# Kernel optimization log

Hardware: AMD Instinct MI355X
Metric: run time of the kernel (lower is better)

## Reference

```python
import jax, jax.numpy as jnp
import numpy as np

DIM = 1024
NH = 16
HD = DIM // NH  # 64
WINDOW = 8      # window_size; flash window=(WINDOW-1, -1) with causal=True
EPS_NORM = 1e-6


def _rmsnorm(h, w):
    # RMSNorm over last dim (full model dim, applied before head split)
    return h * jax.lax.rsqrt(jnp.mean(h * h, axis=-1, keepdims=True) + EPS_NORM) * w


def _rope(h, cos, sin):
    # h: [bv, L, NH, HD]; cos/sin: [L, HD//2]; torch view-as-complex pairs adjacent elems
    hr = h[..., 0::2]
    hi = h[..., 1::2]
    c = cos[None, :, None, :]
    s = sin[None, :, None, :]
    out_r = hr * c - hi * s
    out_i = hr * s + hi * c
    return jnp.stack([out_r, out_i], axis=-1).reshape(h.shape)


def setup_inputs() -> dict:
    key = jax.random.key(0)
    ks = jax.random.split(key, 8)
    bv, f, nlt = 1, 16, 1472
    b = bv * f
    L = f * nlt
    wscale = DIM ** -0.5
    x = jax.random.normal(ks[0], (b, nlt, DIM), jnp.float32)
    # standard RoPE tables, base 10000, d//2 frequencies
    pos = jnp.arange(L, dtype=jnp.float32)[:, None]
    inv_freq = 1.0 / (10000.0 ** (jnp.arange(HD // 2, dtype=jnp.float32) / (HD // 2)))
    ang = pos * inv_freq[None, :]
    inp = {
        'x': x,
        'freqs_cos': jnp.cos(ang),
        'freqs_sin': jnp.sin(ang),
        'q_w': jax.random.normal(ks[1], (DIM, DIM), jnp.float32) * wscale,
        'q_b': jnp.zeros((DIM,), jnp.float32),
        'k_w': jax.random.normal(ks[2], (DIM, DIM), jnp.float32) * wscale,
        'k_b': jnp.zeros((DIM,), jnp.float32),
        'v_w': jax.random.normal(ks[3], (DIM, DIM), jnp.float32) * wscale,
        'v_b': jnp.zeros((DIM,), jnp.float32),
        'o_w': jax.random.normal(ks[4], (DIM, DIM), jnp.float32) * wscale,
        'o_b': jnp.zeros((DIM,), jnp.float32),
        'norm_q_w': jnp.ones((DIM,), jnp.float32),
        'norm_k_w': jnp.ones((DIM,), jnp.float32),
        'bv': 1,
        'f': 16,
        'nlt': 1472,
    }
    return inp


def reference(x, freqs_cos, freqs_sin, q_w, q_b, k_w, k_b, v_w, v_b, o_w, o_b,
              norm_q_w, norm_k_w, bv, f, nlt):
    b, s = x.shape[:2]  # b = bv*f, s = nlt
    q = _rmsnorm(x @ q_w.T + q_b, norm_q_w)
    k = _rmsnorm(x @ k_w.T + k_b, norm_k_w)
    v = (x @ v_w.T + v_b).reshape(bv, f, s, NH, HD)
    # RoPE over flattened (frame, token) positions
    q4 = q.reshape(bv, f * s, NH, HD)
    k4 = k.reshape(bv, f * s, NH, HD)
    qr = _rope(q4, freqs_cos, freqs_sin)
    kr = _rope(k4, freqs_cos, freqs_sin)
    # temporal layout: [bv*nlt, f, NH, HD] (attend over frames per latent token)
    qr = qr.reshape(bv, f, s, NH, HD).transpose(0, 2, 1, 3, 4).reshape(bv * s, f, NH, HD)
    kr = kr.reshape(bv, f, s, NH, HD).transpose(0, 2, 1, 3, 4).reshape(bv * s, f, NH, HD)
    vr = v.transpose(0, 2, 1, 3, 4).reshape(bv * s, f, NH, HD)
    # causal sliding-window mask over frames: j <= i and i - j < WINDOW
    fi = jnp.arange(f)
    mask = (fi[None, :] <= fi[:, None]) & (fi[:, None] - fi[None, :] < WINDOW)  # [f, f]
    scores = jnp.einsum('bqhd,bkhd->bhqk', qr, kr) / np.float32(np.sqrt(HD))
    scores = jnp.where(mask[None, None], scores, jnp.float32(-1e30))
    attn = jax.nn.softmax(scores, axis=-1)
    o = jnp.einsum('bhqk,bkhd->bqhd', attn, vr)  # [bv*nlt, f, NH, HD]
    o = o.reshape(bv, s, f, NH, HD).transpose(0, 2, 1, 3, 4).reshape(bv * f, s, DIM)
    return o @ o_w.T + o_b
```

## Files before the change

kernel.cpp:

```cpp
#include <hip/hip_runtime.h>
#include <hip/hip_bf16.h>
#include <math.h>

typedef __bf16 bf16;
typedef bf16 bf16x8 __attribute__((ext_vector_type(8)));
typedef bf16 bf16x4 __attribute__((ext_vector_type(4)));
typedef float f32x4 __attribute__((ext_vector_type(4)));

#define NFRM 16
#define SEQ  1472
#define TOK  (NFRM * SEQ)
#define DIM_ 1024
#define NH_  16
#define HD_  64
#define KROW 1032


__device__ __forceinline__ void load_lds_16B(const void* g, void* l) {
  __builtin_amdgcn_global_load_lds(
      (const __attribute__((address_space(1))) unsigned int*)g,
      (__attribute__((address_space(3))) unsigned int*)l,
      16, 0, 0);
}

__global__ __launch_bounds__(256) void cvt_bf16(const float* __restrict__ s,
                                                bf16* __restrict__ d, int n) {
  size_t i = ((size_t)blockIdx.x * 256 + threadIdx.x) * 8;
  if (i >= (size_t)n) return;
  const int r   = (int)(i >> 10);
  const int col = (int)(i & 1023);
  const int f   = r / SEQ;
  const int t   = r - f * SEQ;
  const size_t o = ((size_t)(t * 16 + f) << 10) + col;
  f32x4 a = *(const f32x4*)(s + i);
  f32x4 b = *(const f32x4*)(s + i + 4);
  bf16x8 v;
  v[0] = (bf16)a[0]; v[1] = (bf16)a[1]; v[2] = (bf16)a[2]; v[3] = (bf16)a[3];
  v[4] = (bf16)b[0]; v[5] = (bf16)b[1]; v[6] = (bf16)b[2]; v[7] = (bf16)b[3];
  *(bf16x8*)(d + o) = v;
}

__global__ __launch_bounds__(256) void cvt_w4(
    const float* __restrict__ w0, const float* __restrict__ w1,
    const float* __restrict__ w2, const float* __restrict__ w3,
    bf16* __restrict__ d0, bf16* __restrict__ d1,
    bf16* __restrict__ d2, bf16* __restrict__ d3) {
  const int z = blockIdx.y;
  const float* s = (z == 0) ? w0 : (z == 1) ? w1 : (z == 2) ? w2 : w3;
  bf16* d       = (z == 0) ? d0 : (z == 1) ? d1 : (z == 2) ? d2 : d3;
  size_t i = ((size_t)blockIdx.x * 256 + threadIdx.x) * 8;
  f32x4 a = *(const f32x4*)(s + i);
  f32x4 b = *(const f32x4*)(s + i + 4);
  bf16x8 o;
  o[0] = (bf16)a[0]; o[1] = (bf16)a[1]; o[2] = (bf16)a[2]; o[3] = (bf16)a[3];
  o[4] = (bf16)b[0]; o[5] = (bf16)b[1]; o[6] = (bf16)b[2]; o[7] = (bf16)b[3];
  *(bf16x8*)(d + i) = o;
}

__device__ __forceinline__ void swz368(int h, int& bx, int& by) {
  const int s = (h & 7) * 46 + (h >> 3);
  bx = s >> 2;
  by = s & 3;
}

template <typename OutT, int OMAP>
__device__ __forceinline__ void gemm256_body(const bf16* __restrict__ A,
                                             const bf16* __restrict__ B,
                                             const float* __restrict__ bias,
                                             OutT* __restrict__ C,
                                             bf16* lds, int bx, int by) {
  const int tid  = threadIdx.x;
  const int w    = tid >> 6;
  const int lane = tid & 63;
  const int am0  = bx * 256;
  const int bn0  = by * 256;

  const int rstep = w * 8 + (lane >> 3);
  const int jsrc  = ((lane & 7) ^ ((lane >> 3) & 7)) * 8;
  const int arb[4] = {0, 128, 64, 192};
  const bf16* srcp[8];
  int dstoff[8];
#pragma unroll
  for (int s = 0; s < 4; ++s) {
    srcp[s]   = B + (size_t)(bn0 + s * 64 + rstep) * DIM_ + jsrc;
    dstoff[s] = 32768 + s * 8192 + w * 1024;
    srcp[4 + s]   = A + (size_t)(am0 + arb[s] + rstep) * DIM_ + jsrc;
    dstoff[4 + s] = arb[s] * 128 + w * 1024;
  }

  const int wr   = w >> 2;
  const int wc   = w & 3;
  const int frow = lane & 15;
  const int g    = lane >> 4;
  const int sw   = (frow & 7) << 4;
  const int e0   = (g * 16) ^ sw;
  const int e1   = (g * 16 + 64) ^ sw;
  const int aA   = (wr * 128 + frow) * 128;
  const int bB   = 32768 + (wc * 64 + frow) * 128;

  f32x4 acc[8][4];
#pragma unroll
  for (int i = 0; i < 8; ++i)
#pragma unroll
    for (int j = 0; j < 4; ++j) {
      f32x4 z = {0.f, 0.f, 0.f, 0.f};
      acc[i][j] = z;
    }

  char* ldsc = (char*)lds;

#pragma unroll
  for (int s = 0; s < 8; ++s) load_lds_16B(srcp[s], ldsc + dstoff[s]);

#pragma unroll 1
  for (int it = 0; it < 8; ++it) {
#pragma unroll
    for (int half = 0; half < 2; ++half) {
      const int kt   = it * 2 + half;
      const int cur  = half ? 65536 : 0;
      const int nxt  = half ? 0 : 65536;
      const int kpre = (kt < 15) ? (kt + 1) * 64 : 15 * 64;

      asm volatile("s_waitcnt vmcnt(2)" ::: "memory");
      asm volatile("s_barrier" ::: "memory");
#pragma unroll
      for (int s = 0; s < 4; ++s)
        load_lds_16B(srcp[s] + kpre, ldsc + nxt + dstoff[s]);

      bf16x8 bfv[4][2];
#pragma unroll
      for (int j = 0; j < 4; ++j) {
        bfv[j][0] = *(const bf16x8*)(ldsc + cur + bB + j * 2048 + e0);
        bfv[j][1] = *(const bf16x8*)(ldsc + cur + bB + j * 2048 + e1);
      }

#pragma unroll
      for (int p = 0; p < 4; ++p) {
        if (p == 1) {
          load_lds_16B(srcp[4] + kpre, ldsc + nxt + dstoff[4]);
          load_lds_16B(srcp[5] + kpre, ldsc + nxt + dstoff[5]);
        }
        if (p == 2) {
          asm volatile("s_waitcnt vmcnt(6)" ::: "memory");
          asm volatile("s_barrier" ::: "memory");
          load_lds_16B(srcp[6] + kpre, ldsc + nxt + dstoff[6]);
          load_lds_16B(srcp[7] + kpre, ldsc + nxt + dstoff[7]);
        }
        bf16x8 af[2][2];
#pragma unroll
        for (int ii = 0; ii < 2; ++ii) {
          const int i = p * 2 + ii;
          af[ii][0] = *(const bf16x8*)(ldsc + cur + aA + i * 2048 + e0);
          af[ii][1] = *(const bf16x8*)(ldsc + cur + aA + i * 2048 + e1);
        }
        __builtin_amdgcn_s_setprio(1);
#pragma unroll
        for (int ii = 0; ii < 2; ++ii) {
          const int i = p * 2 + ii;
#pragma unroll
          for (int j = 0; j < 4; ++j) {
            acc[i][j] = __builtin_amdgcn_mfma_f32_16x16x32_bf16(
                af[ii][0], bfv[j][0], acc[i][j], 0, 0, 0);
            acc[i][j] = __builtin_amdgcn_mfma_f32_16x16x32_bf16(
                af[ii][1], bfv[j][1], acc[i][j], 0, 0, 0);
          }
        }
        __builtin_amdgcn_s_setprio(0);
      }
    }
  }

  const int cl = lane & 15;
  const int rq = g * 4;
#pragma unroll
  for (int j = 0; j < 4; ++j) {
    const int nc   = bn0 + wc * 64 + j * 16 + cl;
    const float bb = bias[nc];
#pragma unroll
    for (int i = 0; i < 8; ++i) {
#pragma unroll
      for (int r = 0; r < 4; ++r) {
        const int rowp = am0 + wr * 128 + i * 16 + rq + r;
        const size_t mr = (OMAP == 1)
            ? ((size_t)(rowp & 15) * SEQ + (rowp >> 4))
            : (size_t)rowp;
        C[mr * DIM_ + nc] = (OutT)(acc[i][j][r] + bb);
      }
    }
  }
}

__global__ __launch_bounds__(512, 2) void gemm_qkv(
    const bf16* __restrict__ A,
    const bf16* __restrict__ Bq, const bf16* __restrict__ Bk,
    const bf16* __restrict__ Bv,
    const float* __restrict__ bq, const float* __restrict__ bk,
    const float* __restrict__ bv,
    bf16* __restrict__ Cq, bf16* __restrict__ Ck, bf16* __restrict__ Cv) {
  __shared__ __align__(16) bf16 lds[65536];
  const int z = blockIdx.z;
  const bf16* B    = (z == 0) ? Bq : (z == 1) ? Bk : Bv;
  const float* bia = (z == 0) ? bq : (z == 1) ? bk : bv;
  bf16* C          = (z == 0) ? Cq : (z == 1) ? Ck : Cv;
  int bx, by;
  swz368(blockIdx.y * 92 + blockIdx.x, bx, by);
  gemm256_body<bf16, 0>(A, B, bia, C, lds, bx, by);
}

__global__ __launch_bounds__(512, 2) void gemm_out(
    const bf16* __restrict__ A, const bf16* __restrict__ B,
    const float* __restrict__ bias, float* __restrict__ C) {
  __shared__ __align__(16) bf16 lds[65536];
  int bx, by;
  swz368(blockIdx.y * 92 + blockIdx.x, bx, by);
  gemm256_body<float, 1>(A, B, bias, C, lds, bx, by);
}

__global__ __launch_bounds__(512, 4) void attn_win(
    const bf16* __restrict__ q, const bf16* __restrict__ k,
    const bf16* __restrict__ v, bf16* __restrict__ o,
    const float* __restrict__ nqw, const float* __restrict__ nkw,
    const float* __restrict__ fcos, const float* __restrict__ fsin) {
  __shared__ __align__(16) bf16 ks[16 * KROW];
  __shared__ __align__(16) bf16 xs[16 * KROW];
  __shared__ __align__(16) bf16 ps[16 * 256];
  const int t    = blockIdx.x;
  const int tid  = threadIdx.x;
  const int wave = tid >> 6, lane = tid & 63;
  const size_t tb = (size_t)t * (16 * DIM_);

  const bf16* vg = v + tb + (size_t)tid * 32;
  bf16x8 vr0 = *(const bf16x8*)(vg);
  bf16x8 vr1 = *(const bf16x8*)(vg + 8);
  bf16x8 vr2 = *(const bf16x8*)(vg + 16);
  bf16x8 vr3 = *(const bf16x8*)(vg + 24);

#pragma unroll
  for (int i = 0; i < 4; ++i) {
    const int j = wave * 4 + i;
    const int r = j >> 1, half = j & 1;
    const size_t g = tb + (size_t)r * DIM_ + half * 512 + lane * 8;
    load_lds_16B(k + g, ks + r * KROW + half * 512);
    load_lds_16B(q + g, xs + r * KROW + half * 512);
  }
  __syncthreads();

#pragma unroll
  for (int i = 0; i < 4; ++i) {
    const int m  = wave * 4 + i;
    const int fr = m & 15;
    bf16* rowp = ((m < 16) ? xs : ks) + fr * KROW;
    const float* nw = (m < 16) ? nqw : nkw;
    bf16x8 a = *(const bf16x8*)(rowp + lane * 8);
    bf16x8 b = *(const bf16x8*)(rowp + 512 + lane * 8);
    float xa[8], xb[8];
    float ssq = 0.f;
#pragma unroll
    for (int e = 0; e < 8; ++e) {
      xa[e] = (float)a[e]; xb[e] = (float)b[e];
      ssq += xa[e] * xa[e] + xb[e] * xb[e];
    }
#pragma unroll
    for (int off = 32; off > 0; off >>= 1) ssq += __shfl_xor(ssq, off);
    const float rs = rsqrtf(ssq * (1.0f / 1024.0f) + 1e-6f);
    float wA[8], wB[8];
    f32x4 w0 = *(const f32x4*)(nw + lane * 8);
    f32x4 w1 = *(const f32x4*)(nw + lane * 8 + 4);
    f32x4 w2 = *(const f32x4*)(nw + 512 + lane * 8);
    f32x4 w3 = *(const f32x4*)(nw + 512 + lane * 8 + 4);
#pragma unroll
    for (int e = 0; e < 4; ++e) {
      wA[e] = w0[e]; wA[4 + e] = w1[e];
      wB[e] = w2[e]; wB[4 + e] = w3[e];
    }
    const size_t pos = (size_t)fr * SEQ + t;
    f32x4 cc = *(const f32x4*)(fcos + pos * 32 + (lane & 7) * 4);
    f32x4 sn = *(const f32x4*)(fsin + pos * 32 + (lane & 7) * 4);
    bf16x8 oa, ob;
#pragma unroll
    for (int p = 0; p < 4; ++p) {
      const float a0 = xa[2 * p] * rs * wA[2 * p];
      const float a1 = xa[2 * p + 1] * rs * wA[2 * p + 1];
      const float b0 = xb[2 * p] * rs * wB[2 * p];
      const float b1 = xb[2 * p + 1] * rs * wB[2 * p + 1];
      oa[2 * p]     = (bf16)(a0 * cc[p] - a1 * sn[p]);
      oa[2 * p + 1] = (bf16)(a0 * sn[p] + a1 * cc[p]);
      ob[2 * p]     = (bf16)(b0 * cc[p] - b1 * sn[p]);
      ob[2 * p + 1] = (bf16)(b0 * sn[p] + b1 * cc[p]);
    }
    *(bf16x8*)(rowp + lane * 8)       = oa;
    *(bf16x8*)(rowp + 512 + lane * 8) = ob;
  }
  __syncthreads();

  const int fl  = lane & 15;
  const int kq  = (lane >> 4) * 8;
#pragma unroll
  for (int hh = 0; hh < 2; ++hh) {
    const int h = wave * 2 + hh;
    const int qo = fl * KROW + h * HD_ + kq;
    bf16x8 aq0 = *(const bf16x8*)(xs + qo);
    bf16x8 aq1 = *(const bf16x8*)(xs + qo + 32);
    bf16x8 bk0 = *(const bf16x8*)(ks + qo);
    bf16x8 bk1 = *(const bf16x8*)(ks + qo + 32);
    f32x4 sc = {0.f, 0.f, 0.f, 0.f};
    sc = __builtin_amdgcn_mfma_f32_16x16x32_bf16(aq0, bk0, sc, 0, 0, 0);
    sc = __builtin_amdgcn_mfma_f32_16x16x32_bf16(aq1, bk1, sc, 0, 0, 0);
#pragma unroll
    for (int r = 0; r < 4; ++r) {
      const int row = (lane >> 4) * 4 + r;
      const bool valid = (fl <= row) && (row - fl < 8);
      float s = valid ? sc[r] * 0.125f : -1e30f;
      float m = s;
#pragma unroll
      for (int off = 8; off > 0; off >>= 1) m = fmaxf(m, __shfl_xor(m, off));
      const float e = __expf(s - m);
      float su = e;
#pragma unroll
      for (int off = 8; off > 0; off >>= 1) su += __shfl_xor(su, off);
      ps[h * 256 + row * 16 + fl] = (bf16)(e / su);
    }
  }
  __syncthreads();

  {
    bf16* vd = xs + (tid >> 5) * KROW + (tid & 31) * 32;
    *(bf16x8*)(vd)      = vr0;
    *(bf16x8*)(vd + 8)  = vr1;
    *(bf16x8*)(vd + 16) = vr2;
    *(bf16x8*)(vd + 24) = vr3;
  }
  __syncthreads();

  const int h3 = tid >> 5;
  const int dc = (tid >> 2) & 7;
  const int fg = tid & 3;
  bf16x8 pr[8];
#pragma unroll
  for (int i = 0; i < 4; ++i) {
    pr[2 * i]     = *(const bf16x8*)(ps + h3 * 256 + (fg * 4 + i) * 16);
    pr[2 * i + 1] = *(const bf16x8*)(ps + h3 * 256 + (fg * 4 + i) * 16 + 8);
  }
  float acc[4][8];
#pragma unroll
  for (int i = 0; i < 4; ++i)
#pragma unroll
    for (int d = 0; d < 8; ++d) acc[i][d] = 0.f;

  const bf16* vb = xs + h3 * HD_ + dc * 8;
#pragma unroll
  for (int fk2 = 0; fk2 < 16; ++fk2) {
    bf16x8 vv8 = *(const bf16x8*)(vb + fk2 * KROW);
    float vf[8];
#pragma unroll
    for (int d = 0; d < 8; ++d) vf[d] = (float)vv8[d];
#pragma unroll
    for (int i = 0; i < 4; ++i) {
      const float pp = (float)((fk2 < 8) ? pr[2 * i][fk2] : pr[2 * i + 1][fk2 - 8]);
#pragma unroll
      for (int d = 0; d < 8; ++d) acc[i][d] += pp * vf[d];
    }
  }
#pragma unroll
  for (int i = 0; i < 4; ++i) {
    bf16x8 ov;
#pragma unroll
    for (int d = 0; d < 8; ++d) ov[d] = (bf16)acc[i][d];
    *(bf16x8*)(o + tb + (size_t)(fg * 4 + i) * DIM_ + h3 * HD_ + dc * 8) = ov;
  }
}

extern "C" void kernel_launch(void* const* d_in, const int* in_sizes, int n_in,
                              void* d_out, int out_size, void* d_ws,
                              size_t ws_size, hipStream_t stream) {
  const float* x    = (const float*)d_in[0];
  const float* fcos = (const float*)d_in[1];
  const float* fsin = (const float*)d_in[2];
  const float* q_w  = (const float*)d_in[3];
  const float* q_b  = (const float*)d_in[4];
  const float* k_w  = (const float*)d_in[5];
  const float* k_b  = (const float*)d_in[6];
  const float* v_w  = (const float*)d_in[7];
  const float* v_b  = (const float*)d_in[8];
  const float* o_w  = (const float*)d_in[9];
  const float* o_b  = (const float*)d_in[10];
  const float* nqw  = (const float*)d_in[11];
  const float* nkw  = (const float*)d_in[12];
  float* out = (float*)d_out;

  char* ws = (char*)d_ws;
  const size_t SZ  = (size_t)TOK * DIM_ * 2;
  const size_t WSZ = (size_t)DIM_ * DIM_ * 2;
  bf16* xb = (bf16*)(ws);
  bf16* wq = (bf16*)(ws + SZ);
  bf16* wk = (bf16*)(ws + SZ + WSZ);
  bf16* wv = (bf16*)(ws + SZ + 2 * WSZ);
  bf16* wo = (bf16*)(ws + SZ + 3 * WSZ);
  bf16* qq = (bf16*)(ws + SZ + 4 * WSZ);
  bf16* kk = (bf16*)(ws + SZ + 4 * WSZ + SZ);
  bf16* vv = (bf16*)(ws + SZ + 4 * WSZ + 2 * SZ);
  bf16* om = xb;

  const int NTOT = TOK * DIM_;
  const int NW   = DIM_ * DIM_;

  cvt_bf16<<<NTOT / 2048, 256, 0, stream>>>(x, xb, NTOT);
  cvt_w4<<<dim3(NW / 2048, 4), 256, 0, stream>>>(q_w, k_w, v_w, o_w,
                                                 wq, wk, wv, wo);

  dim3 gq(TOK / 256, DIM_ / 256, 3);
  gemm_qkv<<<gq, 512, 0, stream>>>(xb, wq, wk, wv, q_b, k_b, v_b, qq, kk, vv);

  attn_win<<<SEQ, 512, 0, stream>>>(qq, kk, vv, om, nqw, nkw, fcos, fsin);

  gemm_out<<<dim3(TOK / 256, DIM_ / 256), 512, 0, stream>>>(om, wo, o_b, out);
}
```

Measured before the change: 505.3 us.

## Use 128x128 tiles for output GEMM and unify QKV tile swizzle

Replaces the 256x256 output-projection GEMM (368 blocks of 512 threads) with a dedicated 128x128-tile kernel using 256 threads, 32 KB LDS double-buffered and a split A/B prefetch schedule, giving 1472 blocks and up to 3 blocks per CU. This targets poor wave quantization and tail effects when only 368 large tiles run on a 256-CU device. The QKV GEMM now swizzles across all three projections in one flattened index so that tiles sharing the same A rows are scheduled close together for L2 reuse. The cost is lower per-block arithmetic intensity and more global traffic in the output GEMM.

Measured after the change: 502.0 us. No clear change (-0.7%).

```diff
diff --git a/kernel.cpp b/kernel.cpp
--- a/kernel.cpp
+++ b/kernel.cpp
@@ -57,17 +57,10 @@
   *(bf16x8*)(d + i) = o;
 }
 
-__device__ __forceinline__ void swz368(int h, int& bx, int& by) {
-  const int s = (h & 7) * 46 + (h >> 3);
-  bx = s >> 2;
-  by = s & 3;
-}
-
-template <typename OutT, int OMAP>
 __device__ __forceinline__ void gemm256_body(const bf16* __restrict__ A,
                                              const bf16* __restrict__ B,
                                              const float* __restrict__ bias,
-                                             OutT* __restrict__ C,
+                                             bf16* __restrict__ C,
                                              bf16* lds, int bx, int by) {
   const int tid  = threadIdx.x;
   const int w    = tid >> 6;
@@ -180,11 +173,8 @@
     for (int i = 0; i < 8; ++i) {
 #pragma unroll
       for (int r = 0; r < 4; ++r) {
-        const int rowp = am0 + wr * 128 + i * 16 + rq + r;
-        const size_t mr = (OMAP == 1)
-            ? ((size_t)(rowp & 15) * SEQ + (rowp >> 4))
-            : (size_t)rowp;
-        C[mr * DIM_ + nc] = (OutT)(acc[i][j][r] + bb);
+        const size_t mr = (size_t)(am0 + wr * 128 + i * 16 + rq + r);
+        C[mr * DIM_ + nc] = (bf16)(acc[i][j][r] + bb);
       }
     }
   }
@@ -198,22 +188,116 @@
     const float* __restrict__ bv,
     bf16* __restrict__ Cq, bf16* __restrict__ Ck, bf16* __restrict__ Cv) {
   __shared__ __align__(16) bf16 lds[65536];
-  const int z = blockIdx.z;
+  const int h  = blockIdx.z * 368 + blockIdx.y * 92 + blockIdx.x;
+  const int s  = (h & 7) * 138 + (h >> 3);
+  const int bx = s / 12;
+  const int rr = s - bx * 12;
+  const int z  = rr >> 2;
+  const int by = rr & 3;
   const bf16* B    = (z == 0) ? Bq : (z == 1) ? Bk : Bv;
   const float* bia = (z == 0) ? bq : (z == 1) ? bk : bv;
   bf16* C          = (z == 0) ? Cq : (z == 1) ? Ck : Cv;
-  int bx, by;
-  swz368(blockIdx.y * 92 + blockIdx.x, bx, by);
-  gemm256_body<bf16, 0>(A, B, bia, C, lds, bx, by);
-}
-
-__global__ __launch_bounds__(512, 2) void gemm_out(
+  gemm256_body(A, B, bia, C, lds, bx, by);
+}
+
+__global__ __launch_bounds__(256, 3) void gemm_out(
     const bf16* __restrict__ A, const bf16* __restrict__ B,
     const float* __restrict__ bias, float* __restrict__ C) {
-  __shared__ __align__(16) bf16 lds[65536];
-  int bx, by;
-  swz368(blockIdx.y * 92 + blockIdx.x, bx, by);
-  gemm256_body<float, 1>(A, B, bias, C, lds, bx, by);
+  __shared__ __align__(16) bf16 lds[16384];
+  const int h  = blockIdx.y * 184 + blockIdx.x;
+  const int s  = (h & 7) * 184 + (h >> 3);
+  const int bx = s >> 3, by = s & 7;
+  const int am0 = bx * 128, bn0 = by * 128;
+  const int tid = threadIdx.x, w = tid >> 6, lane = tid & 63;
+
+  const int rstep = tid >> 2;
+  const int csw   = ((tid & 3) ^ (rstep & 3)) * 8;
+  const bf16* srcp[4];
+  int dstoff[4];
+  srcp[0] = A + (size_t)(am0 + rstep) * DIM_ + csw;       dstoff[0] = 0;
+  srcp[1] = A + (size_t)(am0 + 64 + rstep) * DIM_ + csw;  dstoff[1] = 4096;
+  srcp[2] = B + (size_t)(bn0 + rstep) * DIM_ + csw;       dstoff[2] = 8192;
+  srcp[3] = B + (size_t)(bn0 + 64 + rstep) * DIM_ + csw;  dstoff[3] = 12288;
+#pragma unroll
+  for (int q = 0; q < 4; ++q) dstoff[q] += w * 1024;
+
+  const int frow = lane & 15;
+  const int g    = lane >> 4;
+  const int swr  = (g ^ (frow & 3)) * 16;
+  const int aoff = (w * 32 + frow) * 64 + swr;
+  const int boff = 8192 + frow * 64 + swr;
+
+  f32x4 acc[2][8];
+#pragma unroll
+  for (int i = 0; i < 2; ++i)
+#pragma unroll
+    for (int j = 0; j < 8; ++j) {
+      f32x4 z = {0.f, 0.f, 0.f, 0.f};
+      acc[i][j] = z;
+    }
+
+  char* ldsc = (char*)lds;
+#pragma unroll
+  for (int q = 0; q < 4; ++q) load_lds_16B(srcp[q], ldsc + dstoff[q]);
+
+  bf16x8 af[2], bfv[4];
+#pragma unroll 1
+  for (int kt = 0; kt < 32; ++kt) {
+    const int cur  = (kt & 1) << 14;
+    const int nxt  = ((kt & 1) ^ 1) << 14;
+    const int kpre = (kt < 31) ? (kt + 1) * 32 : 31 * 32;
+
+    asm volatile("s_waitcnt vmcnt(1)" ::: "memory");
+    asm volatile("s_barrier" ::: "memory");
+    load_lds_16B(srcp[0] + kpre, ldsc + nxt + dstoff[0]);
+    load_lds_16B(srcp[1] + kpre, ldsc + nxt + dstoff[1]);
+    af[0] = *(const bf16x8*)(ldsc + cur + aoff);
+    af[1] = *(const bf16x8*)(ldsc + cur + aoff + 1024);
+#pragma unroll
+    for (int j = 0; j < 4; ++j)
+      bfv[j] = *(const bf16x8*)(ldsc + cur + boff + j * 1024);
+    __builtin_amdgcn_s_setprio(1);
+#pragma unroll
+    for (int i = 0; i < 2; ++i)
+#pragma unroll
+      for (int j = 0; j < 4; ++j)
+        acc[i][j] = __builtin_amdgcn_mfma_f32_16x16x32_bf16(af[i], bfv[j],
+                                                            acc[i][j], 0, 0, 0);
+    __builtin_amdgcn_s_setprio(0);
+
+    asm volatile("s_waitcnt vmcnt(2)" ::: "memory");
+    asm volatile("s_barrier" ::: "memory");
+    load_lds_16B(srcp[2] + kpre, ldsc + nxt + dstoff[2]);
+    load_lds_16B(srcp[3] + kpre, ldsc + nxt + dstoff[3]);
+#pragma unroll
+    for (int j = 0; j < 4; ++j)
+      bfv[j] = *(const bf16x8*)(ldsc + cur + boff + 4096 + j * 1024);
+    __builtin_amdgcn_s_setprio(1);
+#pragma unroll
+    for (int i = 0; i < 2; ++i)
+#pragma unroll
+      for (int j = 0; j < 4; ++j)
+        acc[i][4 + j] = __builtin_amdgcn_mfma_f32_16x16x32_bf16(
+            af[i], bfv[j], acc[i][4 + j], 0, 0, 0);
+    __builtin_amdgcn_s_setprio(0);
+  }
+
+  const int cl = lane & 15;
+  const int rq = g * 4;
+#pragma unroll
+  for (int j = 0; j < 8; ++j) {
+    const int nc   = bn0 + j * 16 + cl;
+    const float bb = bias[nc];
+#pragma unroll
+    for (int i = 0; i < 2; ++i) {
+#pragma unroll
+      for (int r = 0; r < 4; ++r) {
+        const int rowp = am0 + w * 32 + i * 16 + rq + r;
+        const size_t mr = (size_t)(rowp & 15) * SEQ + (rowp >> 4);
+        C[mr * DIM_ + nc] = acc[i][j][r] + bb;
+      }
+    }
+  }
 }
 
 __global__ __launch_bounds__(512, 4) void attn_win(
@@ -413,5 +497,5 @@
 
   attn_win<<<SEQ, 512, 0, stream>>>(qq, kk, vv, om, nqw, nkw, fcos, fsin);
 
-  gemm_out<<<dim3(TOK / 256, DIM_ / 256), 512, 0, stream>>>(om, wo, o_b, out);
-}
+  gemm_out<<<dim3(TOK / 128, DIM_ / 128), 256, 0, stream>>>(om, wo, o_b, out);
+}
```
